# Optimization experiments

Hardware: AMD Instinct MI355X
Metric: run time of the kernel (lower is better)

The kernel has to match this reference:

```python
import jax, jax.numpy as jnp
import numpy as np

N_NODES = 100000
N_EDGES = 1600000
D_IN = 64
D_HID = 64


def setup_inputs() -> dict:
    key = jax.random.key(0)
    k1, k2, k3, k4, k5 = jax.random.split(key, 5)
    x = jax.random.normal(k1, (N_NODES, D_IN), dtype=jnp.float32)
    edge_index = jax.random.randint(k2, (2, N_EDGES), 0, N_NODES, dtype=jnp.int64)
    edge_weight = jax.random.uniform(k3, (N_EDGES,), dtype=jnp.float32)
    # GCNConv glorot-initialized linear weights (bias=False)
    s0 = (6.0 / (D_IN + D_HID)) ** 0.5
    W0 = jax.random.uniform(k4, (D_IN, D_HID), minval=-s0, maxval=s0, dtype=jnp.float32)
    s1 = (6.0 / (D_HID + D_HID)) ** 0.5
    W1 = jax.random.uniform(k5, (D_HID, D_HID), minval=-s1, maxval=s1, dtype=jnp.float32)
    return {"x": x, "edge_index": edge_index, "edge_weight": edge_weight, "W0": W0, "W1": W1}


def _gcn_layer(x, W, src, dst, edge_weight, deg_inv_sqrt, n_nodes):
    # h = X W  (bias=False)
    h = x @ W  # [N, D]
    # symmetric normalization including self-loops (weight 1)
    norm = deg_inv_sqrt[src] * edge_weight * deg_inv_sqrt[dst]  # [E]
    # gather src features, scale, scatter-sum at dst
    agg = jax.ops.segment_sum(norm[:, None] * h[src], dst, num_segments=n_nodes)
    # self-loop contribution: norm_ii = deg_inv_sqrt[i]^2 * 1
    agg = agg + (deg_inv_sqrt * deg_inv_sqrt)[:, None] * h
    return jax.nn.relu(agg)  # dropout is identity in eval mode


def reference(x, edge_index, edge_weight, W0, W1):
    src, dst = edge_index[0], edge_index[1]
    # degree with self-loops (self-loop weight = 1), aggregated at dst (source_to_target flow)
    deg = jax.ops.segment_sum(edge_weight, dst, num_segments=N_NODES) + 1.0
    deg_inv_sqrt = jax.lax.rsqrt(deg)
    x = _gcn_layer(x, W0, src, dst, edge_weight, deg_inv_sqrt, N_NODES)
    x = _gcn_layer(x, W1, src, dst, edge_weight, deg_inv_sqrt, N_NODES)
    return x
```

## Files before the change

kernel.cpp:

```cpp
#include <hip/hip_runtime.h>
#include <hip/hip_fp16.h>

#define D 64
#define BSH 9
#define BSZ (1 << BSH)
#define PB 4096
#define CAPR 18432
#define CAPU (2 * CAPR)
#define SCAP 9216

__global__ __launch_bounds__(256) void initcur(int* __restrict__ ccur, int nbuck) {
    int t = threadIdx.x;
    if (t < nbuck) ccur[t] = t * CAPR;
}

__global__ __launch_bounds__(512) void bucket1(const int* __restrict__ src,
                                               const int* __restrict__ dst,
                                               const float* __restrict__ ew,
                                               int* __restrict__ ccur,
                                               int2* __restrict__ pairs2,
                                               int E, int nbuck) {
    __shared__ int hist[512];
    __shared__ int lbase[512];
    __shared__ int gbase[512];
    __shared__ int w0s[PB];
    __shared__ int w1s[PB];
    __shared__ unsigned char bids[PB];
    int t = threadIdx.x;
    hist[t] = 0;
    __syncthreads();
    int e0 = blockIdx.x * PB;
    int cnt = min(PB, E - e0);
    int b[8], lr[8], w0[8], w1[8];
    int i8 = t * 8;
    bool full8 = (i8 + 8 <= cnt);
    if (full8) {
        int4   sa = *(const int4*)&src[e0 + i8];
        int4   sb = *(const int4*)&src[e0 + i8 + 4];
        int4   da = *(const int4*)&dst[e0 + i8];
        int4   db = *(const int4*)&dst[e0 + i8 + 4];
        float4 wa = *(const float4*)&ew[e0 + i8];
        float4 wb = *(const float4*)&ew[e0 + i8 + 4];
        int ss[8] = {sa.x, sa.y, sa.z, sa.w, sb.x, sb.y, sb.z, sb.w};
        int ds[8] = {da.x, da.y, da.z, da.w, db.x, db.y, db.z, db.w};
        float wv[8] = {wa.x, wa.y, wa.z, wa.w, wb.x, wb.y, wb.z, wb.w};
#pragma unroll
        for (int k = 0; k < 8; ++k) {
            b[k]  = ds[k] >> BSH;
            w0[k] = ss[k] | ((ds[k] & (BSZ - 1)) << 17);
            w1[k] = __float_as_int(wv[k]);
            lr[k] = atomicAdd(&hist[b[k]], 1);
        }
    } else {
#pragma unroll
        for (int k = 0; k < 8; ++k) {
            int idx = i8 + k;
            if (idx < cnt) {
                int d = dst[e0 + idx];
                b[k]  = d >> BSH;
                w0[k] = src[e0 + idx] | ((d & (BSZ - 1)) << 17);
                w1[k] = __float_as_int(ew[e0 + idx]);
                lr[k] = atomicAdd(&hist[b[k]], 1);
            }
        }
    }
    __syncthreads();
    int hv = hist[t];
    lbase[t] = hv;
    __syncthreads();
    for (int off = 1; off < 512; off <<= 1) {
        int u = (t >= off) ? lbase[t - off] : 0;
        __syncthreads();
        lbase[t] += u;
        __syncthreads();
    }
    int excl = lbase[t] - hv;
    __syncthreads();
    lbase[t] = excl;
    if (t < nbuck && hv > 0) gbase[t] = atomicAdd(&ccur[t], hv);
    __syncthreads();
#pragma unroll
    for (int k = 0; k < 8; ++k) {
        int idx = i8 + k;
        if (idx < cnt) {
            int slot = lbase[b[k]] + lr[k];
            w0s[slot] = w0[k];
            w1s[slot] = w1[k];
            bids[slot] = (unsigned char)b[k];
        }
    }
    __syncthreads();
    for (int i = t; i < cnt; i += 512) {
        int bb = bids[i];
        int pos = gbase[bb] + (i - lbase[bb]);
        pairs2[pos] = make_int2(w0s[i], w1s[i]);
    }
}

__global__ __launch_bounds__(512) void sort2(int2* __restrict__ pairs2,
                                             unsigned int* __restrict__ pairsU,
                                             const int* __restrict__ ccur,
                                             int2* __restrict__ rng,
                                             float* __restrict__ dis,
                                             int N, int nbuck) {
    __shared__ int2 se[SCAP];
    __shared__ int cnt[512];
    __shared__ float sdeg[512];
    __shared__ int lb[512];
    __shared__ int nbase[512];
    int b = blockIdx.x;
    int t = threadIdx.x;
    int baseR = b * CAPR;
    int baseU = b * CAPU;
    int cntb = min(ccur[b] - baseR, SCAP);
    for (int i = t; i < cntb; i += 512) se[i] = pairs2[baseR + i];
    cnt[t] = 0;
    sdeg[t] = 0.0f;
    __syncthreads();
    for (int i = t; i < cntb; i += 512) {
        int2 p = se[i];
        int dl = (p.x >> 17) & (BSZ - 1);
        int lr = atomicAdd(&cnt[dl], 1);
        atomicAdd(&sdeg[dl], __int_as_float(p.y));
        se[i].x = p.x | (lr << 26);
    }
    __syncthreads();
    int node = (b << BSH) + t;
    int pc = (node < N) ? ((cnt[t] + 1 + 31) & ~31) : 0;
    lb[t] = pc;
    __syncthreads();
    for (int off = 1; off < 512; off <<= 1) {
        int u = (t >= off) ? lb[t - off] : 0;
        __syncthreads();
        lb[t] += u;
        __syncthreads();
    }
    int excl = lb[t] - pc;
    int totalPad = lb[511];
    float dloc = rsqrtf(sdeg[t] + 1.0f);
    __syncthreads();
    sdeg[t]  = dloc;
    nbase[t] = baseU + excl;
    if (node < N) {
        rng[node] = make_int2(baseU + excl, baseU + excl + pc);
        dis[node] = dloc;
    }
    for (int i = t; i < totalPad; i += 512) pairsU[baseU + i] = 0u;
    __syncthreads();
    for (int i = t; i < cntb; i += 512) {
        int2 p = se[i];
        int dl = (p.x >> 17) & (BSZ - 1);
        int s  = p.x & 0x1FFFF;
        int rank = ((unsigned int)p.x) >> 26;
        int pos = nbase[dl] + rank;
        float w = __int_as_float(p.y) * sdeg[dl];
        unsigned int h = (unsigned int)__half_as_ushort(__float2half_rn(w));
        pairsU[pos] = ((unsigned int)s << 15) | ((h + 1u) >> 1);
    }
    if (node < N) {
        unsigned int h = (unsigned int)__half_as_ushort(__float2half_rn(dloc));
        pairsU[nbase[t] + cnt[t]] = ((unsigned int)node << 15) | ((h + 1u) >> 1);
    }
}

__global__ __launch_bounds__(256) void gemm64h(const float* __restrict__ X,
                                               const float* __restrict__ W,
                                               const float* __restrict__ dis,
                                               __half* __restrict__ Hb, int n) {
    __shared__ float Ws[64 * 64];
    __shared__ float Xs[16 * 64];
    for (int t = threadIdx.x; t < 64 * 64; t += 256) Ws[t] = W[t];
    int row0 = blockIdx.x * 16;
    for (int t = threadIdx.x; t < 16 * 64; t += 256) {
        int r = row0 + (t >> 6);
        Xs[t] = (r < n) ? X[r * 64 + (t & 63)] : 0.0f;
    }
    __syncthreads();
    int r  = threadIdx.x >> 4;
    int jc = (threadIdx.x & 15) * 4;
    float4 acc = make_float4(0.f, 0.f, 0.f, 0.f);
#pragma unroll
    for (int k = 0; k < 64; ++k) {
        float xv = Xs[r * 64 + k];
        float4 w = *(const float4*)&Ws[k * 64 + jc];
        acc.x += xv * w.x; acc.y += xv * w.y; acc.z += xv * w.z; acc.w += xv * w.w;
    }
    int rr = row0 + r;
    if (rr < n) {
        float ds = dis[rr];
        ushort4 pk;
        pk.x = __half_as_ushort(__float2half(ds * acc.x));
        pk.y = __half_as_ushort(__float2half(ds * acc.y));
        pk.z = __half_as_ushort(__float2half(ds * acc.z));
        pk.w = __half_as_ushort(__float2half(ds * acc.w));
        *(ushort4*)&Hb[rr * 64 + jc] = pk;
    }
}

__global__ __launch_bounds__(256) void gather64(const unsigned int* __restrict__ pairs,
                                                const int2* __restrict__ rng,
                                                const __half* __restrict__ Hb,
                                                float* __restrict__ OUT, int N) {
    int node = blockIdx.x * 4 + (threadIdx.x >> 6);
    if (node >= N) return;
    int lane = threadIdx.x & 63;
    int g    = lane >> 3;
    int fl   = (lane & 7) * 8;
    int2 be = rng[node];
    __half2 z = __float2half2_rn(0.0f);
    __half2 a0[4] = {z, z, z, z};
    __half2 a1[4] = {z, z, z, z};
    __half2 a2[4] = {z, z, z, z};
    __half2 a3[4] = {z, z, z, z};
    for (int e = be.x; e < be.y; e += 32) {
        unsigned int pv = pairs[e + (lane & 31)];
        unsigned int q0 = __shfl(pv, g, 64);
        unsigned int q1 = __shfl(pv, g + 8, 64);
        unsigned int q2 = __shfl(pv, g + 16, 64);
        unsigned int q3 = __shfl(pv, g + 24, 64);
        uint4 r0 = *(const uint4*)(Hb + (size_t)(q0 >> 15) * 64 + fl);
        uint4 r1 = *(const uint4*)(Hb + (size_t)(q1 >> 15) * 64 + fl);
        uint4 r2 = *(const uint4*)(Hb + (size_t)(q2 >> 15) * 64 + fl);
        uint4 r3 = *(const uint4*)(Hb + (size_t)(q3 >> 15) * 64 + fl);
        __half2 w0 = __half2half2(__ushort_as_half((unsigned short)((q0 & 0x7FFFu) << 1)));
        __half2 w1 = __half2half2(__ushort_as_half((unsigned short)((q1 & 0x7FFFu) << 1)));
        __half2 w2 = __half2half2(__ushort_as_half((unsigned short)((q2 & 0x7FFFu) << 1)));
        __half2 w3 = __half2half2(__ushort_as_half((unsigned short)((q3 & 0x7FFFu) << 1)));
        const __half2* h0 = (const __half2*)&r0;
        const __half2* h1 = (const __half2*)&r1;
        const __half2* h2 = (const __half2*)&r2;
        const __half2* h3 = (const __half2*)&r3;
#pragma unroll
        for (int k = 0; k < 4; ++k) {
            a0[k] = __hfma2(w0, h0[k], a0[k]);
            a1[k] = __hfma2(w1, h1[k], a1[k]);
            a2[k] = __hfma2(w2, h2[k], a2[k]);
            a3[k] = __hfma2(w3, h3[k], a3[k]);
        }
    }
    __half2 a[4];
#pragma unroll
    for (int k = 0; k < 4; ++k)
        a[k] = __hadd2(__hadd2(a0[k], a1[k]), __hadd2(a2[k], a3[k]));
#pragma unroll
    for (int m = 8; m < 64; m <<= 1) {
#pragma unroll
        for (int k = 0; k < 4; ++k) {
            unsigned u = __shfl_xor(*(unsigned*)&a[k], m, 64);
            a[k] = __hadd2(a[k], *(__half2*)&u);
        }
    }
    if (g < 2) {
        int o = g * 2;
        float2 f0 = __half22float2(a[o]);
        float2 f1 = __half22float2(a[o + 1]);
        float4 vv;
        vv.x = fmaxf(f0.x, 0.0f);
        vv.y = fmaxf(f0.y, 0.0f);
        vv.z = fmaxf(f1.x, 0.0f);
        vv.w = fmaxf(f1.y, 0.0f);
        *(float4*)&OUT[node * 64 + fl + g * 4] = vv;
    }
}

extern "C" void kernel_launch(void* const* d_in, const int* in_sizes, int n_in,
                              void* d_out, int out_size, void* d_ws, size_t ws_size,
                              hipStream_t stream) {
    const float* x  = (const float*)d_in[0];
    const int*   ei = (const int*)d_in[1];
    const float* ew = (const float*)d_in[2];
    const float* W0 = (const float*)d_in[3];
    const float* W1 = (const float*)d_in[4];
    float* out = (float*)d_out;

    const int N = in_sizes[0] / D;
    const int E = in_sizes[2];
    const int* src = ei;
    const int* dst = ei + E;

    const int nbuck = (N + BSZ - 1) >> BSH;
    const int Na = (N + 1 + 255) & ~255;

    float* dis     = (float*)d_ws;
    int2*  rng     = (int2*)((int*)d_ws + Na);
    int*   ccur    = (int*)d_ws + 3 * Na;
    int2*  pairs2  = (int2*)((int*)d_ws + 3 * Na + 1024);
    unsigned int* pairsU = (unsigned int*)pairs2;
    __half* Hb     = (__half*)((int*)d_ws + 3 * Na + 1024 + (size_t)nbuck * CAPU);

    const int nb1 = (E + PB - 1) / PB;

    initcur<<<1, 256, 0, stream>>>(ccur, nbuck);
    bucket1<<<nb1, 512, 0, stream>>>(src, dst, ew, ccur, pairs2, E, nbuck);
    sort2<<<nbuck, 512, 0, stream>>>(pairs2, pairsU, ccur, rng, dis, N, nbuck);

    const int gemm_grid   = (N + 15) / 16;
    const int gather_grid = (N + 3) / 4;

    gemm64h<<<gemm_grid, 256, 0, stream>>>(x, W0, dis, Hb, N);
    gather64<<<gather_grid, 256, 0, stream>>>(pairsU, rng, Hb, out, N);

    gemm64h<<<gemm_grid, 256, 0, stream>>>(out, W1, dis, Hb, N);
    gather64<<<gather_grid, 256, 0, stream>>>(pairsU, rng, Hb, out, N);
}
```

Before: 195.8 us.

## Split CSR into fixed 32-slot fast segments plus overflow extension array

Replaces the per-bucket prefix-scan padded CSR with a fixed 32-entry slot per node, addressable directly from the node id, plus a global overflow array allocated by atomic add for nodes with more than 31 edges. The gather loads the first 32 entries without first reading a range, and the block-wide scan in the sort kernel goes away. CAPR shrinks, so the bucket staging memory is smaller. The trade-off is that every node is zero-padded to 32 slots, and high-degree nodes take an extra indirection through the extension range. The overflow counter reuses ccur[255], which is safe only while nbuck stays below 256.

```diff
diff --git a/kernel.cpp b/kernel.cpp
--- a/kernel.cpp
+++ b/kernel.cpp
@@ -5,13 +5,15 @@
 #define BSH 9
 #define BSZ (1 << BSH)
 #define PB 4096
-#define CAPR 18432
+#define CAPR 10240
 #define CAPU (2 * CAPR)
+#define FASTU (BSZ * 32)
 #define SCAP 9216
 
 __global__ __launch_bounds__(256) void initcur(int* __restrict__ ccur, int nbuck) {
     int t = threadIdx.x;
     if (t < nbuck) ccur[t] = t * CAPR;
+    if (t == 255) ccur[255] = 0;
 }
 
 __global__ __launch_bounds__(512) void bucket1(const int* __restrict__ src,
@@ -98,16 +100,17 @@
 }
 
 __global__ __launch_bounds__(512) void sort2(int2* __restrict__ pairs2,
-                                             unsigned int* __restrict__ pairsU,
+                                             unsigned int* __restrict__ fastU,
                                              const int* __restrict__ ccur,
-                                             int2* __restrict__ rng,
+                                             int2* __restrict__ extRng,
+                                             unsigned int* __restrict__ extU,
+                                             int* __restrict__ gext,
                                              float* __restrict__ dis,
                                              int N, int nbuck) {
     __shared__ int2 se[SCAP];
     __shared__ int cnt[512];
     __shared__ float sdeg[512];
-    __shared__ int lb[512];
-    __shared__ int nbase[512];
+    __shared__ int ebase[512];
     int b = blockIdx.x;
     int t = threadIdx.x;
     int baseR = b * CAPR;
@@ -126,40 +129,38 @@
     }
     __syncthreads();
     int node = (b << BSH) + t;
-    int pc = (node < N) ? ((cnt[t] + 1 + 31) & ~31) : 0;
-    lb[t] = pc;
-    __syncthreads();
-    for (int off = 1; off < 512; off <<= 1) {
-        int u = (t >= off) ? lb[t - off] : 0;
-        __syncthreads();
-        lb[t] += u;
-        __syncthreads();
-    }
-    int excl = lb[t] - pc;
-    int totalPad = lb[511];
+    int cntv = cnt[t];
+    int pc = (node < N) ? ((cntv + 1 + 31) & ~31) : 0;
+    int extLen = (pc > 32) ? (pc - 32) : 0;
+    int extBase = 0;
+    if (extLen > 0) extBase = atomicAdd(gext, extLen);
     float dloc = rsqrtf(sdeg[t] + 1.0f);
     __syncthreads();
     sdeg[t]  = dloc;
-    nbase[t] = baseU + excl;
+    ebase[t] = extBase;
     if (node < N) {
-        rng[node] = make_int2(baseU + excl, baseU + excl + pc);
-        dis[node] = dloc;
-    }
-    for (int i = t; i < totalPad; i += 512) pairsU[baseU + i] = 0u;
+        extRng[node] = make_int2(extBase, extBase + extLen);
+        dis[node]    = dloc;
+    }
+    for (int i = t; i < FASTU; i += 512) fastU[baseU + i] = 0u;
     __syncthreads();
     for (int i = t; i < cntb; i += 512) {
         int2 p = se[i];
         int dl = (p.x >> 17) & (BSZ - 1);
         int s  = p.x & 0x1FFFF;
         int rank = ((unsigned int)p.x) >> 26;
-        int pos = nbase[dl] + rank;
         float w = __int_as_float(p.y) * sdeg[dl];
         unsigned int h = (unsigned int)__half_as_ushort(__float2half_rn(w));
-        pairsU[pos] = ((unsigned int)s << 15) | ((h + 1u) >> 1);
+        unsigned int packed = ((unsigned int)s << 15) | ((h + 1u) >> 1);
+        if (rank < 32) fastU[baseU + dl * 32 + rank] = packed;
+        else           extU[ebase[dl] + rank - 32]   = packed;
     }
     if (node < N) {
         unsigned int h = (unsigned int)__half_as_ushort(__float2half_rn(dloc));
-        pairsU[nbase[t] + cnt[t]] = ((unsigned int)node << 15) | ((h + 1u) >> 1);
+        unsigned int selfp = ((unsigned int)node << 15) | ((h + 1u) >> 1);
+        if (cntv < 32) fastU[baseU + t * 32 + cntv] = selfp;
+        else           extU[extBase + cntv - 32]    = selfp;
+        for (int i = cntv + 1 - 32; i < extLen; ++i) extU[extBase + i] = 0u;
     }
 }
 
@@ -197,8 +198,38 @@
     }
 }
 
-__global__ __launch_bounds__(256) void gather64(const unsigned int* __restrict__ pairs,
-                                                const int2* __restrict__ rng,
+__device__ __forceinline__ void acc_group(unsigned int pv, int g, int fl,
+                                          const __half* __restrict__ Hb,
+                                          __half2 a0[4], __half2 a1[4],
+                                          __half2 a2[4], __half2 a3[4]) {
+    unsigned int q0 = __shfl(pv, g, 64);
+    unsigned int q1 = __shfl(pv, g + 8, 64);
+    unsigned int q2 = __shfl(pv, g + 16, 64);
+    unsigned int q3 = __shfl(pv, g + 24, 64);
+    uint4 r0 = *(const uint4*)(Hb + (size_t)(q0 >> 15) * 64 + fl);
+    uint4 r1 = *(const uint4*)(Hb + (size_t)(q1 >> 15) * 64 + fl);
+    uint4 r2 = *(const uint4*)(Hb + (size_t)(q2 >> 15) * 64 + fl);
+    uint4 r3 = *(const uint4*)(Hb + (size_t)(q3 >> 15) * 64 + fl);
+    __half2 w0 = __half2half2(__ushort_as_half((unsigned short)((q0 & 0x7FFFu) << 1)));
+    __half2 w1 = __half2half2(__ushort_as_half((unsigned short)((q1 & 0x7FFFu) << 1)));
+    __half2 w2 = __half2half2(__ushort_as_half((unsigned short)((q2 & 0x7FFFu) << 1)));
+    __half2 w3 = __half2half2(__ushort_as_half((unsigned short)((q3 & 0x7FFFu) << 1)));
+    const __half2* h0 = (const __half2*)&r0;
+    const __half2* h1 = (const __half2*)&r1;
+    const __half2* h2 = (const __half2*)&r2;
+    const __half2* h3 = (const __half2*)&r3;
+#pragma unroll
+    for (int k = 0; k < 4; ++k) {
+        a0[k] = __hfma2(w0, h0[k], a0[k]);
+        a1[k] = __hfma2(w1, h1[k], a1[k]);
+        a2[k] = __hfma2(w2, h2[k], a2[k]);
+        a3[k] = __hfma2(w3, h3[k], a3[k]);
+    }
+}
+
+__global__ __launch_bounds__(256) void gather64(const unsigned int* __restrict__ fastU,
+                                                const unsigned int* __restrict__ extU,
+                                                const int2* __restrict__ extRng,
                                                 const __half* __restrict__ Hb,
                                                 float* __restrict__ OUT, int N) {
     int node = blockIdx.x * 4 + (threadIdx.x >> 6);
@@ -206,38 +237,18 @@
     int lane = threadIdx.x & 63;
     int g    = lane >> 3;
     int fl   = (lane & 7) * 8;
-    int2 be = rng[node];
+    int l31  = lane & 31;
+    int fbase = (node >> BSH) * CAPU + (node & (BSZ - 1)) * 32;
+    unsigned int pv = fastU[fbase + l31];
+    int2 er = extRng[node];
     __half2 z = __float2half2_rn(0.0f);
     __half2 a0[4] = {z, z, z, z};
     __half2 a1[4] = {z, z, z, z};
     __half2 a2[4] = {z, z, z, z};
     __half2 a3[4] = {z, z, z, z};
-    for (int e = be.x; e < be.y; e += 32) {
-        unsigned int pv = pairs[e + (lane & 31)];
-        unsigned int q0 = __shfl(pv, g, 64);
-        unsigned int q1 = __shfl(pv, g + 8, 64);
-        unsigned int q2 = __shfl(pv, g + 16, 64);
-        unsigned int q3 = __shfl(pv, g + 24, 64);
-        uint4 r0 = *(const uint4*)(Hb + (size_t)(q0 >> 15) * 64 + fl);
-        uint4 r1 = *(const uint4*)(Hb + (size_t)(q1 >> 15) * 64 + fl);
-        uint4 r2 = *(const uint4*)(Hb + (size_t)(q2 >> 15) * 64 + fl);
-        uint4 r3 = *(const uint4*)(Hb + (size_t)(q3 >> 15) * 64 + fl);
-        __half2 w0 = __half2half2(__ushort_as_half((unsigned short)((q0 & 0x7FFFu) << 1)));
-        __half2 w1 = __half2half2(__ushort_as_half((unsigned short)((q1 & 0x7FFFu) << 1)));
-        __half2 w2 = __half2half2(__ushort_as_half((unsigned short)((q2 & 0x7FFFu) << 1)));
-        __half2 w3 = __half2half2(__ushort_as_half((unsigned short)((q3 & 0x7FFFu) << 1)));
-        const __half2* h0 = (const __half2*)&r0;
-        const __half2* h1 = (const __half2*)&r1;
-        const __half2* h2 = (const __half2*)&r2;
-        const __half2* h3 = (const __half2*)&r3;
-#pragma unroll
-        for (int k = 0; k < 4; ++k) {
-            a0[k] = __hfma2(w0, h0[k], a0[k]);
-            a1[k] = __hfma2(w1, h1[k], a1[k]);
-            a2[k] = __hfma2(w2, h2[k], a2[k]);
-            a3[k] = __hfma2(w3, h3[k], a3[k]);
-        }
-    }
+    acc_group(pv, g, fl, Hb, a0, a1, a2, a3);
+    for (int e = er.x; e < er.y; e += 32)
+        acc_group(extU[e + l31], g, fl, Hb, a0, a1, a2, a3);
     __half2 a[4];
 #pragma unroll
     for (int k = 0; k < 4; ++k)
@@ -282,24 +293,26 @@
     const int Na = (N + 1 + 255) & ~255;
 
     float* dis     = (float*)d_ws;
-    int2*  rng     = (int2*)((int*)d_ws + Na);
+    int2*  extRng  = (int2*)((int*)d_ws + Na);
     int*   ccur    = (int*)d_ws + 3 * Na;
     int2*  pairs2  = (int2*)((int*)d_ws + 3 * Na + 1024);
-    unsigned int* pairsU = (unsigned int*)pairs2;
+    unsigned int* fastU = (unsigned int*)pairs2;
     __half* Hb     = (__half*)((int*)d_ws + 3 * Na + 1024 + (size_t)nbuck * CAPU);
+    unsigned int* extU = (unsigned int*)((__half*)Hb + (size_t)N * D);
 
     const int nb1 = (E + PB - 1) / PB;
 
     initcur<<<1, 256, 0, stream>>>(ccur, nbuck);
     bucket1<<<nb1, 512, 0, stream>>>(src, dst, ew, ccur, pairs2, E, nbuck);
-    sort2<<<nbuck, 512, 0, stream>>>(pairs2, pairsU, ccur, rng, dis, N, nbuck);
+    sort2<<<nbuck, 512, 0, stream>>>(pairs2, fastU, ccur, extRng, extU,
+                                     ccur + 255, dis, N, nbuck);
 
     const int gemm_grid   = (N + 15) / 16;
     const int gather_grid = (N + 3) / 4;
 
     gemm64h<<<gemm_grid, 256, 0, stream>>>(x, W0, dis, Hb, N);
-    gather64<<<gather_grid, 256, 0, stream>>>(pairsU, rng, Hb, out, N);
+    gather64<<<gather_grid, 256, 0, stream>>>(fastU, extU, extRng, Hb, out, N);
 
     gemm64h<<<gemm_grid, 256, 0, stream>>>(out, W1, dis, Hb, N);
-    gather64<<<gather_grid, 256, 0, stream>>>(pairsU, rng, Hb, out, N);
-}
+    gather64<<<gather_grid, 256, 0, stream>>>(fastU, extU, extRng, Hb, out, N);
+}
```

After: 190.9 us. 2.5% less time.
